# Kernel optimization log

Hardware: AMD Instinct MI355X
Metric: run time of the kernel (lower is better)

## Reference

```python
import jax, jax.numpy as jnp
import numpy as np

B, S, D, E = 4, 2048, 512, 32

def setup_inputs() -> dict:
    key = jax.random.key(0)
    k1, k2, k3 = jax.random.split(key, 3)
    x = jax.random.normal(k1, (B, S, D), dtype=jnp.float32)
    # glorot-ish scaling for weights
    gate_w = jax.random.normal(k2, (D, E), dtype=jnp.float32) * (1.0 / np.sqrt(D))
    gate_b = jnp.zeros((E,), dtype=jnp.float32)
    expert_w = jax.random.normal(k3, (E, D, D), dtype=jnp.float32) * (1.0 / np.sqrt(D))
    return {"x": x, "gate_w": gate_w, "gate_b": gate_b, "expert_w": expert_w}

def reference(x, gate_w, gate_b, expert_w):
    # gate_scores: [B,S,E] (context=None -> route on x itself)
    gate = jax.nn.softmax(jnp.einsum('bsd,de->bse', x, gate_w) + gate_b, axis=-1)
    # Dense soft-MoE: sum_e gate[b,s,e] * (x[b,s,:] @ expert_w[e])
    # Single einsum avoids materializing the [B,S,E,D] intermediate.
    out = jnp.einsum('bse,bsd,edf->bsf', gate, x, expert_w)
    return out
```

## Files before the change

### kernel.cpp

```cpp
#include <hip/hip_runtime.h>

#define TOK 8192
#define DIM 512
#define NE  32
#define KTOT (NE * DIM)

#define BM 128
#define BN 128
#define BK 64

typedef float f32x4 __attribute__((ext_vector_type(4)));
typedef short s16x8 __attribute__((ext_vector_type(8)));

typedef const void __attribute__((address_space(1)))* gp1_t;
typedef void __attribute__((address_space(3)))* lp3_t;

__device__ __forceinline__ void gl_lds16(const void* g, void* l) {
    __builtin_amdgcn_global_load_lds((gp1_t)g, (lp3_t)l, 16, 0, 0);
}

__device__ __forceinline__ ushort f2bf(float f) {
    unsigned u = __builtin_bit_cast(unsigned, f);
    unsigned r = (u + 0x7fffu + ((u >> 16) & 1u)) >> 16;
    return (ushort)r;
}

__global__ __launch_bounds__(256) void k_prep(const float* __restrict__ w,
                                              ushort* __restrict__ wt,
                                              const float* __restrict__ x,
                                              const float* __restrict__ gw,
                                              const float* __restrict__ gb,
                                              float* __restrict__ G,
                                              ushort* __restrict__ xb) {
    __shared__ __align__(16) char smem[64 * 65 * 4];
    const int bx = blockIdx.x;
    const int tid = threadIdx.x;
    if (bx < 2048) {
        float (*tile)[65] = (float(*)[65])smem;
        const int e = bx >> 6;
        const int f0 = ((bx >> 3) & 7) * 64;
        const int d0 = (bx & 7) * 64;
        const float* we = w + (size_t)e * DIM * DIM;

        const int tq = tid & 15, td = tid >> 4;
#pragma unroll
        for (int r = 0; r < 4; ++r) {
            const int d = td + 16 * r;
            const float4 v = *(const float4*)(we + (size_t)(d0 + d) * DIM + f0 + tq * 4);
            tile[d][tq * 4 + 0] = v.x;
            tile[d][tq * 4 + 1] = v.y;
            tile[d][tq * 4 + 2] = v.z;
            tile[d][tq * 4 + 3] = v.w;
        }
        __syncthreads();

        const int tx = tid & 7, ty = tid >> 3;
#pragma unroll
        for (int h = 0; h < 2; ++h) {
            const int f = ty + 32 * h;
            ushort8_tag: ;
            union { ushort u[8]; s16x8 v; } o;
#pragma unroll
            for (int j = 0; j < 8; ++j)
                o.u[j] = f2bf(tile[tx * 8 + j][f]);
            *(s16x8*)(wt + (size_t)(f0 + f) * KTOT + e * DIM + d0 + tx * 8) = o.v;
        }
    } else {
        float* xs = (float*)smem;
        const int t0 = (bx - 2048) * 8;
        const float* xBase = x + (size_t)t0 * DIM;
#pragma unroll
        for (int k = 0; k < 4; ++k) {
            int i4 = (k * 256 + tid) * 4;
            float4 v = *(const float4*)(xBase + i4);
            xs[i4 + 0] = v.x; xs[i4 + 1] = v.y; xs[i4 + 2] = v.z; xs[i4 + 3] = v.w;
            ushort4 o;
            o.x = f2bf(v.x); o.y = f2bf(v.y); o.z = f2bf(v.z); o.w = f2bf(v.w);
            *(ushort4*)(xb + (size_t)t0 * DIM + i4) = o;
        }
        __syncthreads();
        const int tok = tid >> 5;
        const int e = tid & 31;
        float l = gb[e];
        const float* xr = xs + tok * DIM;
#pragma unroll 8
        for (int d = 0; d < DIM; ++d)
            l += xr[d] * gw[d * NE + e];
        float mx = l;
#pragma unroll
        for (int m = 16; m >= 1; m >>= 1) mx = fmaxf(mx, __shfl_xor(mx, m));
        float ex = expf(l - mx);
        float s = ex;
#pragma unroll
        for (int m = 16; m >= 1; m >>= 1) s += __shfl_xor(s, m);
        G[(size_t)(t0 + tok) * NE + e] = ex / s;
    }
}

__global__ __launch_bounds__(512, 2) void k_moe_gemm(const ushort* __restrict__ xb,
                                                     const ushort* __restrict__ wt,
                                                     const float* __restrict__ G,
                                                     float* __restrict__ out0,
                                                     float* __restrict__ out1) {
    __shared__ __align__(16) ushort As[2][BM * BK];
    __shared__ __align__(16) ushort Bs[2][BN * BK];
    __shared__ float Gs[16][BM];

    const int tid = threadIdx.x;
    const int m0 = blockIdx.y * BM;
    const int n0 = blockIdx.x * BN;
    const int e0 = blockIdx.z * 16;
    float* __restrict__ dst = blockIdx.z ? out1 : out0;

    for (int i = tid; i < 16 * BM; i += 512) {
        int e = i >> 7, r = i & 127;
        Gs[e][r] = G[(size_t)(m0 + r) * NE + e0 + e];
    }

    const int lane = tid & 63;
    const int wave = tid >> 6;
    const int wm = (wave & 3) * 32;
    const int wn = (wave >> 2) * 64;
    const int l15 = lane & 15;
    const int q = lane >> 4;
    const int keyR = l15 & 7;

    const int swz0 = ((q) ^ keyR) * 16;
    const int swz1 = ((4 + q) ^ keyR) * 16;
    const int rowA0 = (wm + l15) * 128;
    const int rowA1 = (wm + 16 + l15) * 128;
    const int rowB0 = (wn + l15) * 128;
    const int rowB1 = (wn + 16 + l15) * 128;
    const int rowB2 = (wn + 32 + l15) * 128;
    const int rowB3 = (wn + 48 + l15) * 128;

    const int srow = tid >> 3;
    const int chunk = tid & 7;
    const int scol = ((chunk ^ (srow & 7)) * 8);
    const ushort* aBase = xb + (size_t)(m0 + srow) * DIM + scol;
    const ushort* bBase = wt + (size_t)(n0 + srow) * KTOT + (size_t)e0 * DIM + scol;
    const int ldsOff = tid * 16;

    const f32x4 zv = {0.f, 0.f, 0.f, 0.f};
    f32x4 acc[2][4];
#pragma unroll
    for (int i = 0; i < 2; ++i)
#pragma unroll
        for (int j = 0; j < 4; ++j) acc[i][j] = zv;

    gl_lds16(aBase, (char*)As[0] + ldsOff);
    gl_lds16(aBase + (size_t)64 * DIM, (char*)As[0] + 8192 + ldsOff);
    gl_lds16(bBase, (char*)Bs[0] + ldsOff);
    gl_lds16(bBase + (size_t)64 * KTOT, (char*)Bs[0] + 8192 + ldsOff);
    __syncthreads();

#pragma unroll 1
    for (int kt = 0; kt < 8; ++kt) {
        const char* Ab = (const char*)As[kt & 1];
#pragma unroll 1
        for (int ee = 0; ee < 16; ++ee) {
            const int gn = kt * 16 + ee + 1;
            if (gn < 128) {
                const ushort* bN = bBase + (size_t)(gn & 15) * DIM + (gn >> 4) * BK;
                char* bL = (char*)Bs[gn & 1] + ldsOff;
                gl_lds16(bN, bL);
                gl_lds16(bN + (size_t)64 * KTOT, bL + 8192);
                if (ee == 15) {
                    const ushort* aN = aBase + (kt + 1) * BK;
                    char* aL = (char*)As[(kt + 1) & 1] + ldsOff;
                    gl_lds16(aN, aL);
                    gl_lds16(aN + (size_t)64 * DIM, aL + 8192);
                }
            }

            const char* Bb = (const char*)Bs[ee & 1];
            f32x4 pacc[2][4];
#pragma unroll
            for (int ks = 0; ks < 2; ++ks) {
                const int swz = ks ? swz1 : swz0;
                s16x8 a0 = *(const s16x8*)(Ab + rowA0 + swz);
                s16x8 a1 = *(const s16x8*)(Ab + rowA1 + swz);
                s16x8 b0 = *(const s16x8*)(Bb + rowB0 + swz);
                s16x8 b1 = *(const s16x8*)(Bb + rowB1 + swz);
                s16x8 b2 = *(const s16x8*)(Bb + rowB2 + swz);
                s16x8 b3 = *(const s16x8*)(Bb + rowB3 + swz);
                if (ks == 0) {
                    pacc[0][0] = __builtin_amdgcn_mfma_f32_16x16x32_bf16(a0, b0, zv, 0, 0, 0);
                    pacc[0][1] = __builtin_amdgcn_mfma_f32_16x16x32_bf16(a0, b1, zv, 0, 0, 0);
                    pacc[0][2] = __builtin_amdgcn_mfma_f32_16x16x32_bf16(a0, b2, zv, 0, 0, 0);
                    pacc[0][3] = __builtin_amdgcn_mfma_f32_16x16x32_bf16(a0, b3, zv, 0, 0, 0);
                    pacc[1][0] = __builtin_amdgcn_mfma_f32_16x16x32_bf16(a1, b0, zv, 0, 0, 0);
                    pacc[1][1] = __builtin_amdgcn_mfma_f32_16x16x32_bf16(a1, b1, zv, 0, 0, 0);
                    pacc[1][2] = __builtin_amdgcn_mfma_f32_16x16x32_bf16(a1, b2, zv, 0, 0, 0);
                    pacc[1][3] = __builtin_amdgcn_mfma_f32_16x16x32_bf16(a1, b3, zv, 0, 0, 0);
                } else {
                    pacc[0][0] = __builtin_amdgcn_mfma_f32_16x16x32_bf16(a0, b0, pacc[0][0], 0, 0, 0);
                    pacc[0][1] = __builtin_amdgcn_mfma_f32_16x16x32_bf16(a0, b1, pacc[0][1], 0, 0, 0);
                    pacc[0][2] = __builtin_amdgcn_mfma_f32_16x16x32_bf16(a0, b2, pacc[0][2], 0, 0, 0);
                    pacc[0][3] = __builtin_amdgcn_mfma_f32_16x16x32_bf16(a0, b3, pacc[0][3], 0, 0, 0);
                    pacc[1][0] = __builtin_amdgcn_mfma_f32_16x16x32_bf16(a1, b0, pacc[1][0], 0, 0, 0);
                    pacc[1][1] = __builtin_amdgcn_mfma_f32_16x16x32_bf16(a1, b1, pacc[1][1], 0, 0, 0);
                    pacc[1][2] = __builtin_amdgcn_mfma_f32_16x16x32_bf16(a1, b2, pacc[1][2], 0, 0, 0);
                    pacc[1][3] = __builtin_amdgcn_mfma_f32_16x16x32_bf16(a1, b3, pacc[1][3], 0, 0, 0);
                }
            }

#pragma unroll
            for (int i = 0; i < 2; ++i) {
                const f32x4 gt = *(const f32x4*)&Gs[ee][wm + i * 16 + q * 4];
#pragma unroll
                for (int j = 0; j < 4; ++j) {
                    acc[i][j][0] += gt[0] * pacc[i][j][0];
                    acc[i][j][1] += gt[1] * pacc[i][j][1];
                    acc[i][j][2] += gt[2] * pacc[i][j][2];
                    acc[i][j][3] += gt[3] * pacc[i][j][3];
                }
            }
            __syncthreads();
        }
    }

#pragma unroll
    for (int i = 0; i < 2; ++i) {
        const int tl = m0 + wm + i * 16 + q * 4;
#pragma unroll
        for (int j = 0; j < 4; ++j) {
            const int f = n0 + wn + j * 16 + l15;
            float* p = dst + (size_t)tl * DIM + f;
            p[0 * DIM] = acc[i][j][0];
            p[1 * DIM] = acc[i][j][1];
            p[2 * DIM] = acc[i][j][2];
            p[3 * DIM] = acc[i][j][3];
        }
    }
}

__global__ __launch_bounds__(256) void k_reduce(float* __restrict__ out,
                                                const float* __restrict__ P) {
    int i = (blockIdx.x * 256 + threadIdx.x) * 4;
    float4 a = *(const float4*)(out + i);
    float4 b = *(const float4*)(P + i);
    a.x += b.x; a.y += b.y; a.z += b.z; a.w += b.w;
    *(float4*)(out + i) = a;
}

extern "C" void kernel_launch(void* const* d_in, const int* in_sizes, int n_in,
                              void* d_out, int out_size, void* d_ws, size_t ws_size,
                              hipStream_t stream) {
    const float* x  = (const float*)d_in[0];
    const float* gw = (const float*)d_in[1];
    const float* gb = (const float*)d_in[2];
    const float* w  = (const float*)d_in[3];
    float* out = (float*)d_out;

    char* ws = (char*)d_ws;
    ushort* xb = (ushort*)ws;
    ushort* wt = (ushort*)(ws + (8u << 20));
    float*  G  = (float*)(ws + (24u << 20));
    float*  P  = (float*)(ws + (25u << 20));

    k_prep<<<dim3(2048 + TOK / 8), dim3(256), 0, stream>>>(w, wt, x, gw, gb, G, xb);
    k_moe_gemm<<<dim3(DIM / BN, TOK / BM, 2), dim3(512), 0, stream>>>(xb, wt, G, out, P);
    k_reduce<<<dim3(TOK * DIM / 1024), dim3(256), 0, stream>>>(out, P);
}
```

Before: 261.8 us.

## Fuse prep, GEMM and reduction into one persistent kernel with grid barrier

Merges the weight-transpose/convert, gating softmax, expert GEMM and split-K reduction into a single 512-block kernel. Blocks zero the output, do their share of prep, then meet at a global atomic barrier before the GEMM phase. The two expert halves accumulate into the output with float atomics, which removes the partial buffer and the reduction pass. This saves two kernel launches and the extra partial-buffer traffic, but adds a spin barrier that needs all 512 blocks resident at once, plus atomic contention and nondeterministic summation order.

```diff
diff --git a/kernel.cpp b/kernel.cpp
--- a/kernel.cpp
+++ b/kernel.cpp
@@ -8,6 +8,7 @@
 #define BM 128
 #define BN 128
 #define BK 64
+#define NBLK 512
 
 typedef float f32x4 __attribute__((ext_vector_type(4)));
 typedef short s16x8 __attribute__((ext_vector_type(8)));
@@ -25,53 +26,66 @@
     return (ushort)r;
 }
 
-__global__ __launch_bounds__(256) void k_prep(const float* __restrict__ w,
-                                              ushort* __restrict__ wt,
-                                              const float* __restrict__ x,
-                                              const float* __restrict__ gw,
-                                              const float* __restrict__ gb,
-                                              float* __restrict__ G,
-                                              ushort* __restrict__ xb) {
-    __shared__ __align__(16) char smem[64 * 65 * 4];
-    const int bx = blockIdx.x;
+__global__ __launch_bounds__(512, 2) void k_fused(const float* __restrict__ w,
+                                                  const float* __restrict__ x,
+                                                  const float* __restrict__ gw,
+                                                  const float* __restrict__ gb,
+                                                  ushort* __restrict__ wt,
+                                                  ushort* __restrict__ xb,
+                                                  float* __restrict__ G,
+                                                  float* __restrict__ out,
+                                                  unsigned* __restrict__ bar) {
+    __shared__ __align__(16) char lds[73728];
+
+    const int bid = blockIdx.x;
     const int tid = threadIdx.x;
-    if (bx < 2048) {
-        float (*tile)[65] = (float(*)[65])smem;
-        const int e = bx >> 6;
-        const int f0 = ((bx >> 3) & 7) * 64;
-        const int d0 = (bx & 7) * 64;
-        const float* we = w + (size_t)e * DIM * DIM;
-
+
+    {
+        const float4 z4 = {0.f, 0.f, 0.f, 0.f};
+        float* o = out + (size_t)bid * 8192;
+#pragma unroll
+        for (int r = 0; r < 4; ++r)
+            *(float4*)(o + (size_t)(r * 512 + tid) * 4) = z4;
+    }
+
+    {
+        float (*tile)[65] = (float(*)[65])lds;
         const int tq = tid & 15, td = tid >> 4;
-#pragma unroll
-        for (int r = 0; r < 4; ++r) {
-            const int d = td + 16 * r;
-            const float4 v = *(const float4*)(we + (size_t)(d0 + d) * DIM + f0 + tq * 4);
-            tile[d][tq * 4 + 0] = v.x;
-            tile[d][tq * 4 + 1] = v.y;
-            tile[d][tq * 4 + 2] = v.z;
-            tile[d][tq * 4 + 3] = v.w;
-        }
-        __syncthreads();
-
-        const int tx = tid & 7, ty = tid >> 3;
-#pragma unroll
-        for (int h = 0; h < 2; ++h) {
-            const int f = ty + 32 * h;
-            ushort8_tag: ;
-            union { ushort u[8]; s16x8 v; } o;
+        const int tx = tid & 7,  tf = tid >> 3;
+#pragma unroll 1
+        for (int tt = 0; tt < 4; ++tt) {
+            const int tile_id = bid * 4 + tt;
+            const int e = tile_id >> 6;
+            const int f0 = ((tile_id >> 3) & 7) * 64;
+            const int d0 = (tile_id & 7) * 64;
+            const float* we = w + (size_t)e * DIM * DIM;
+#pragma unroll
+            for (int r = 0; r < 2; ++r) {
+                const int d = td + 32 * r;
+                const float4 v = *(const float4*)(we + (size_t)(d0 + d) * DIM + f0 + tq * 4);
+                tile[d][tq * 4 + 0] = v.x;
+                tile[d][tq * 4 + 1] = v.y;
+                tile[d][tq * 4 + 2] = v.z;
+                tile[d][tq * 4 + 3] = v.w;
+            }
+            __syncthreads();
+            union { ushort u[8]; s16x8 v; } ou;
 #pragma unroll
             for (int j = 0; j < 8; ++j)
-                o.u[j] = f2bf(tile[tx * 8 + j][f]);
-            *(s16x8*)(wt + (size_t)(f0 + f) * KTOT + e * DIM + d0 + tx * 8) = o.v;
-        }
-    } else {
-        float* xs = (float*)smem;
-        const int t0 = (bx - 2048) * 8;
+                ou.u[j] = f2bf(tile[tx * 8 + j][tf]);
+            *(s16x8*)(wt + (size_t)(f0 + tf) * KTOT + e * DIM + d0 + tx * 8) = ou.v;
+            __syncthreads();
+        }
+    }
+
+    {
+        const int u = tid >> 8, t = tid & 255;
+        float* xs = (float*)(lds + 32768) + u * 4096;
+        const int t0 = (bid * 2 + u) * 8;
         const float* xBase = x + (size_t)t0 * DIM;
 #pragma unroll
         for (int k = 0; k < 4; ++k) {
-            int i4 = (k * 256 + tid) * 4;
+            int i4 = (k * 256 + t) * 4;
             float4 v = *(const float4*)(xBase + i4);
             xs[i4 + 0] = v.x; xs[i4 + 1] = v.y; xs[i4 + 2] = v.z; xs[i4 + 3] = v.w;
             ushort4 o;
@@ -79,8 +93,8 @@
             *(ushort4*)(xb + (size_t)t0 * DIM + i4) = o;
         }
         __syncthreads();
-        const int tok = tid >> 5;
-        const int e = tid & 31;
+        const int tok = t >> 5;
+        const int e = t & 31;
         float l = gb[e];
         const float* xr = xs + tok * DIM;
 #pragma unroll 8
@@ -95,22 +109,24 @@
         for (int m = 16; m >= 1; m >>= 1) s += __shfl_xor(s, m);
         G[(size_t)(t0 + tok) * NE + e] = ex / s;
     }
-}
-
-__global__ __launch_bounds__(512, 2) void k_moe_gemm(const ushort* __restrict__ xb,
-                                                     const ushort* __restrict__ wt,
-                                                     const float* __restrict__ G,
-                                                     float* __restrict__ out0,
-                                                     float* __restrict__ out1) {
-    __shared__ __align__(16) ushort As[2][BM * BK];
-    __shared__ __align__(16) ushort Bs[2][BN * BK];
-    __shared__ float Gs[16][BM];
-
-    const int tid = threadIdx.x;
-    const int m0 = blockIdx.y * BM;
-    const int n0 = blockIdx.x * BN;
-    const int e0 = blockIdx.z * 16;
-    float* __restrict__ dst = blockIdx.z ? out1 : out0;
+
+    __syncthreads();
+    if (tid == 0) {
+        __threadfence();
+        __hip_atomic_fetch_add(bar, 1u, __ATOMIC_RELEASE, __HIP_MEMORY_SCOPE_AGENT);
+        while (__hip_atomic_load(bar, __ATOMIC_ACQUIRE, __HIP_MEMORY_SCOPE_AGENT) < NBLK)
+            __builtin_amdgcn_s_sleep(2);
+        __threadfence();
+    }
+    __syncthreads();
+
+    char* As0 = lds;
+    char* Bs0 = lds + 32768;
+    float (*Gs)[BM] = (float(*)[BM])(lds + 65536);
+
+    const int m0 = ((bid >> 2) & 63) * BM;
+    const int n0 = (bid & 3) * BN;
+    const int e0 = (bid >> 8) * 16;
 
     for (int i = tid; i < 16 * BM; i += 512) {
         int e = i >> 7, r = i & 127;
@@ -148,32 +164,32 @@
 #pragma unroll
         for (int j = 0; j < 4; ++j) acc[i][j] = zv;
 
-    gl_lds16(aBase, (char*)As[0] + ldsOff);
-    gl_lds16(aBase + (size_t)64 * DIM, (char*)As[0] + 8192 + ldsOff);
-    gl_lds16(bBase, (char*)Bs[0] + ldsOff);
-    gl_lds16(bBase + (size_t)64 * KTOT, (char*)Bs[0] + 8192 + ldsOff);
+    gl_lds16(aBase, As0 + ldsOff);
+    gl_lds16(aBase + (size_t)64 * DIM, As0 + 8192 + ldsOff);
+    gl_lds16(bBase, Bs0 + ldsOff);
+    gl_lds16(bBase + (size_t)64 * KTOT, Bs0 + 8192 + ldsOff);
     __syncthreads();
 
 #pragma unroll 1
     for (int kt = 0; kt < 8; ++kt) {
-        const char* Ab = (const char*)As[kt & 1];
+        const char* Ab = As0 + ((kt & 1) << 14);
 #pragma unroll 1
         for (int ee = 0; ee < 16; ++ee) {
             const int gn = kt * 16 + ee + 1;
             if (gn < 128) {
                 const ushort* bN = bBase + (size_t)(gn & 15) * DIM + (gn >> 4) * BK;
-                char* bL = (char*)Bs[gn & 1] + ldsOff;
+                char* bL = Bs0 + ((gn & 1) << 14) + ldsOff;
                 gl_lds16(bN, bL);
                 gl_lds16(bN + (size_t)64 * KTOT, bL + 8192);
                 if (ee == 15) {
                     const ushort* aN = aBase + (kt + 1) * BK;
-                    char* aL = (char*)As[(kt + 1) & 1] + ldsOff;
+                    char* aL = As0 + (((kt + 1) & 1) << 14) + ldsOff;
                     gl_lds16(aN, aL);
                     gl_lds16(aN + (size_t)64 * DIM, aL + 8192);
                 }
             }
 
-            const char* Bb = (const char*)Bs[ee & 1];
+            const char* Bb = Bs0 + ((ee & 1) << 14);
             f32x4 pacc[2][4];
 #pragma unroll
             for (int ks = 0; ks < 2; ++ks) {
@@ -226,22 +242,13 @@
 #pragma unroll
         for (int j = 0; j < 4; ++j) {
             const int f = n0 + wn + j * 16 + l15;
-            float* p = dst + (size_t)tl * DIM + f;
-            p[0 * DIM] = acc[i][j][0];
-            p[1 * DIM] = acc[i][j][1];
-            p[2 * DIM] = acc[i][j][2];
-            p[3 * DIM] = acc[i][j][3];
-        }
-    }
-}
-
-__global__ __launch_bounds__(256) void k_reduce(float* __restrict__ out,
-                                                const float* __restrict__ P) {
-    int i = (blockIdx.x * 256 + threadIdx.x) * 4;
-    float4 a = *(const float4*)(out + i);
-    float4 b = *(const float4*)(P + i);
-    a.x += b.x; a.y += b.y; a.z += b.z; a.w += b.w;
-    *(float4*)(out + i) = a;
+            float* p = out + (size_t)tl * DIM + f;
+            unsafeAtomicAdd(p + 0 * DIM, acc[i][j][0]);
+            unsafeAtomicAdd(p + 1 * DIM, acc[i][j][1]);
+            unsafeAtomicAdd(p + 2 * DIM, acc[i][j][2]);
+            unsafeAtomicAdd(p + 3 * DIM, acc[i][j][3]);
+        }
+    }
 }
 
 extern "C" void kernel_launch(void* const* d_in, const int* in_sizes, int n_in,
@@ -257,9 +264,8 @@
     ushort* xb = (ushort*)ws;
     ushort* wt = (ushort*)(ws + (8u << 20));
     float*  G  = (float*)(ws + (24u << 20));
-    float*  P  = (float*)(ws + (25u << 20));
-
-    k_prep<<<dim3(2048 + TOK / 8), dim3(256), 0, stream>>>(w, wt, x, gw, gb, G, xb);
-    k_moe_gemm<<<dim3(DIM / BN, TOK / BM, 2), dim3(512), 0, stream>>>(xb, wt, G, out, P);
-    k_reduce<<<dim3(TOK * DIM / 1024), dim3(256), 0, stream>>>(out, P);
-}
+    unsigned* bar = (unsigned*)(ws + (25u << 20));
+
+    hipMemsetAsync(bar, 0, 4, stream);
+    k_fused<<<dim3(NBLK), dim3(512), 0, stream>>>(w, x, gw, gb, wt, xb, G, out, bar);
+}
```

After: 314.8 us. 1.2x slower.
